# Kernel optimization log

Measured on AMD Instinct MI355X. Metric: run time of the kernel, lower is better.

Reference implementation:

```python
import jax, jax.numpy as jnp
import numpy as np

N, T, NC, D = 256, 20, 1, 32
NF, Q, VSTEPS, HDYN = 16, 32, 10, 256
HDIM = NF * 64           # n_filt * 4**3
DT = 0.1
BETA = 1.0
LOG2PI = float(np.log(2.0 * np.pi))


def conv2d(x, w, b):
    # k=4, s=2, p=1 : halves spatial dims. x: [B,Cin,H,W], w: [Cout,Cin,4,4]
    y = jax.lax.conv_general_dilated(x, w, (2, 2), [(1, 1), (1, 1)],
                                     dimension_numbers=('NCHW', 'OIHW', 'NCHW'))
    return y + b[None, :, None, None]


def deconv2d(x, w, b):
    # stride-2 transposed conv, doubles spatial dims. w: [Cout,Cin,4,4]
    y = jax.lax.conv_transpose(x, w, (2, 2), 'SAME',
                               dimension_numbers=('NCHW', 'OIHW', 'NCHW'))
    return y + b[None, :, None, None]


def encode(x, C1, c1, C2, c2, C3, c3, Wm, bm, Wl, bl):
    h = jax.nn.relu(conv2d(x, C1, c1))
    h = jax.nn.relu(conv2d(h, C2, c2))
    h = jax.nn.relu(conv2d(h, C3, c3))   # [B, 4*NF, 4, 4]
    h = h.reshape(h.shape[0], -1)        # [B, HDIM]
    return h @ Wm + bm, h @ Wl + bl


def setup_inputs() -> dict:
    key = jax.random.key(0)
    ks = jax.random.split(key, 40)
    r = lambda i, shape, s=0.05: s * jax.random.normal(ks[i], shape, jnp.float32)
    inp = {
        'X': jax.random.uniform(ks[0], (N, T, NC, D, D), jnp.float32),
        'eps_s0': jax.random.normal(ks[1], (N, Q), jnp.float32),
        'eps_v0': jax.random.normal(ks[2], (N, Q), jnp.float32),
        # enc_s (input = 1 frame)
        'Cs1': r(3, (NF, NC, 4, 4)), 'cs1': jnp.zeros((NF,)),
        'Cs2': r(4, (2 * NF, NF, 4, 4)), 'cs2': jnp.zeros((2 * NF,)),
        'Cs3': r(5, (4 * NF, 2 * NF, 4, 4)), 'cs3': jnp.zeros((4 * NF,)),
        'Wsm': r(6, (HDIM, Q)), 'bsm': jnp.zeros((Q,)),
        'Wsl': r(7, (HDIM, Q), 0.01), 'bsl': -1.0 * jnp.ones((Q,)),
        # enc_v (input = v_steps frames stacked as channels)
        'Cv1': r(8, (NF, VSTEPS * NC, 4, 4)), 'cv1': jnp.zeros((NF,)),
        'Cv2': r(9, (2 * NF, NF, 4, 4)), 'cv2': jnp.zeros((2 * NF,)),
        'Cv3': r(10, (4 * NF, 2 * NF, 4, 4)), 'cv3': jnp.zeros((4 * NF,)),
        'Wvm': r(11, (HDIM, Q)), 'bvm': jnp.zeros((Q,)),
        'Wvl': r(12, (HDIM, Q), 0.01), 'bvl': -1.0 * jnp.ones((Q,)),
        # dynamics f : R^{2q} -> R^q (tanh MLP)
        'W1': r(13, (2 * Q, HDYN), 0.1), 'b1': jnp.zeros((HDYN,)),
        'W2': r(14, (HDYN, Q), 0.1), 'b2': jnp.zeros((Q,)),
        # fc3 + decoder
        'Wf': r(15, (Q, HDIM)), 'bf': jnp.zeros((HDIM,)),
        'D1': r(16, (2 * NF, 4 * NF, 4, 4)), 'd1': jnp.zeros((2 * NF,)),
        'D2': r(17, (NF, 2 * NF, 4, 4)), 'd2': jnp.zeros((NF,)),
        'D3': r(18, (NC, NF, 4, 4)), 'd3': jnp.zeros((NC,)),
        'Ndata': 10000,
    }
    return inp


def reference(X, eps_s0, eps_v0,
              Cs1, cs1, Cs2, cs2, Cs3, cs3, Wsm, bsm, Wsl, bsl,
              Cv1, cv1, Cv2, cv2, Cv3, cv3, Wvm, bvm, Wvl, bvl,
              W1, b1, W2, b2, Wf, bf, D1, d1, D2, d2, D3, d3, Ndata):
    Nb, Tt = X.shape[0], X.shape[1]
    # ---- encode z0 = [v0, s0]
    s0_mu, s0_lv = encode(X[:, 0], Cs1, cs1, Cs2, cs2, Cs3, cs3, Wsm, bsm, Wsl, bsl)
    xv = X[:, :VSTEPS].reshape(Nb, VSTEPS * NC, D, D)
    v0_mu, v0_lv = encode(xv, Cv1, cv1, Cv2, cv2, Cv3, cv3, Wvm, bvm, Wvl, bvl)
    s0 = s0_mu + eps_s0 * jnp.exp(s0_lv)
    v0 = v0_mu + eps_v0 * jnp.exp(v0_lv)
    # standard-normal density of the base noise (q dims each)
    logp0 = (-0.5 * jnp.sum(eps_s0 ** 2, -1) - 0.5 * Q * LOG2PI) + \
            (-0.5 * jnp.sum(eps_v0 ** 2, -1) - 0.5 * Q * LOG2PI)
    z0 = jnp.concatenate([v0, s0], axis=1)               # [N,2q]
    qz0_m = jnp.concatenate([v0_mu, s0_mu], axis=1)
    qz0_logv = jnp.concatenate([v0_lv, s0_lv], axis=1)

    # ---- augmented ODE rhs: dz = [f(z), v], dlogp = -tr(df/dv)
    # exact trace for the tanh MLP: J = W2^T diag(1-h^2) W1^T, so
    # tr_{i<q} J = (1-h^2) @ c with c_k = sum_{i<q} W1[i,k] * W2[k,i]
    c = jnp.sum(W1[:Q] * W2.T, axis=0)                   # [HDYN]

    def rhs(vs):
        h = jnp.tanh(vs @ W1 + b1)                       # [N,HDYN]
        dv = h @ W2 + b2                                 # [N,q]
        dvs = jnp.concatenate([dv, vs[:, :Q]], axis=1)   # [N,2q]
        tr = (1.0 - h * h) @ c                           # [N]
        return dvs, -tr

    def rk4_step(carry, _):
        z, lp = carry
        k1z, k1l = rhs(z)
        k2z, k2l = rhs(z + 0.5 * DT * k1z)
        k3z, k3l = rhs(z + 0.5 * DT * k2z)
        k4z, k4l = rhs(z + DT * k3z)
        z2 = z + (DT / 6.0) * (k1z + 2 * k2z + 2 * k3z + k4z)
        lp2 = lp + (DT / 6.0) * (k1l + 2 * k2l + 2 * k3l + k4l)
        return (z2, lp2), (z2, lp2)

    (_, _), (zs, lps) = jax.lax.scan(rk4_step, (z0, logp0), None, length=Tt - 1)
    zt = jnp.concatenate([z0[None], zs], axis=0)         # [T,N,2q]
    logp = jnp.concatenate([logp0[None], lps], axis=0)   # [T,N]
    ztL = jnp.transpose(zt, (1, 0, 2))[None]             # [1,N,T,2q] (L=1)
    logpL = logp.T[None]                                 # [1,N,T]

    # ---- decode positions s_t
    s = ztL[..., Q:].reshape(-1, Q) @ Wf + bf            # [N*T, HDIM]
    h = s.reshape(-1, 4 * NF, 4, 4)
    h = jax.nn.relu(deconv2d(h, D1, d1))                 # [N*T,2NF,8,8]
    h = jax.nn.relu(deconv2d(h, D2, d2))                 # [N*T,NF,16,16]
    Xrec = jax.nn.sigmoid(deconv2d(h, D3, d3))           # [N*T,NC,32,32]
    Xrec = Xrec.reshape(1, Nb, Tt, NC, D, D)

    # ---- ELBO
    log_pzt = -0.5 * jnp.sum(ztL ** 2, -1) - Q * LOG2PI  # N(0,I) over 2q dims
    kl_z = (logpL - log_pzt).sum(2).mean(0)              # [N]
    lhood_L = jnp.log(0.001 + Xrec) * X[None] + jnp.log(1.001 - Xrec) * (1.0 - X[None])
    lhood = lhood_L.sum((2, 3, 4, 5)).mean(0)            # [N]
    kl_w = 0.5 * (jnp.sum(W1 ** 2) + jnp.sum(W2 ** 2))
    Nd = jnp.float32(Ndata)
    lh = Nd * lhood.mean()
    klz = Nd * kl_z.mean()
    elbo = lh - klz - BETA * kl_w
    return Xrec, qz0_m, qz0_logv, ztL, elbo, lh, klz, BETA * kl_w


if __name__ == '__main__':
    outs = reference(**setup_inputs())
    print(outs[0].shape, float(outs[4]))
```

## Files before the change

kernel.cpp:

```cpp
#include <hip/hip_runtime.h>
#include <math.h>

#define N_S 256
#define T_S 20
#define D_S 32
#define NF_S 16
#define Q_S 32
#define HDYN_S 256
#define HDIM_S 1024
#define VSTEPS_S 10
#define DT_S 0.1f
#define LOG2PI_F 1.8378770664093453f

#define OUT_XREC 0
#define OUT_QM   5242880
#define OUT_QLV  5259264
#define OUT_ZT   5275648
#define OUT_SCAL 5603328

#define WS_A1    0
#define WS_A3    0
#define WS_WT1   0
#define WS_WT2   32768
#define WS_WT3   40960
#define WS_A2    1048576
#define WS_S0MU  1572864
#define WS_S0LV  1581056
#define WS_V0MU  1589248
#define WS_V0LV  1597440
#define WS_LOGP  1605632
#define WS_LHOOD 1610752
#define WS_KLZ   1611008
#define WS_KLW   1611264
#define WS_TC    1611520
#define TC_S1 (WS_TC + 0)
#define TC_V1 (WS_TC + 256)
#define TC_S2 (WS_TC + 2816)
#define TC_V2 (WS_TC + 11008)
#define TC_S3 (WS_TC + 19200)
#define TC_V3 (WS_TC + 51968)

__device__ inline void enc_tr(const float* __restrict__ src, float* __restrict__ dst,
                              int e, int CI, int CO) {
    int co = e % CO; int r = e / CO; int tap = r & 15; int ci = r >> 4;
    dst[e] = src[(co * CI + ci) * 16 + tap];
}
__device__ inline void dec_tr(const float* __restrict__ src, float* __restrict__ dst,
                              int e, int CI, int CO) {
    int co = e % CO; int r = e / CO; int ci = r % CI; int tap = r / CI;
    dst[e] = src[(co * CI + ci) * 16 + tap];
}

__global__ __launch_bounds__(256) void prep_enc(
    const float* __restrict__ Cs1, const float* __restrict__ Cv1,
    const float* __restrict__ Cs2, const float* __restrict__ Cv2,
    const float* __restrict__ Cs3, const float* __restrict__ Cv3,
    float* __restrict__ ws)
{
    int idx = blockIdx.x * 256 + threadIdx.x;
    if (blockIdx.x == 0) ws[WS_LHOOD + threadIdx.x] = 0.f;
    if (idx < 256)        enc_tr(Cs1, ws + TC_S1, idx,          1, 16);
    else if (idx < 2816)  enc_tr(Cv1, ws + TC_V1, idx - 256,   10, 16);
    else if (idx < 11008) enc_tr(Cs2, ws + TC_S2, idx - 2816,  16, 32);
    else if (idx < 19200) enc_tr(Cv2, ws + TC_V2, idx - 11008, 16, 32);
    else if (idx < 51968) enc_tr(Cs3, ws + TC_S3, idx - 19200, 32, 64);
    else if (idx < 84736) enc_tr(Cv3, ws + TC_V3, idx - 51968, 32, 64);
}

template<int CIN>
__global__ __launch_bounds__(256) void conv1_lds(
    const float* __restrict__ x, const float* __restrict__ wt,
    const float* __restrict__ bias, float* __restrict__ out)
{
    __shared__ float xin[CIN * 630];
    __shared__ float wl[CIN * 256];
    __shared__ float bl[16];
    int b = blockIdx.x, yh = blockIdx.y, t = threadIdx.x;
    for (int e = t; e < CIN * 576; e += 256) {
        int ci = e / 576;
        int r = (e >> 5) - ci * 18;
        int cx = e & 31;
        int gy = yh * 16 - 1 + r;
        float v = (gy >= 0 && gy < 32) ? x[(size_t)b * 20480 + ci * 1024 + gy * 32 + cx] : 0.f;
        xin[ci * 630 + r * 35 + cx + 1] = v;
    }
    for (int e = t; e < CIN * 18; e += 256) {
        int ci = e / 18, r = e - ci * 18;
        xin[ci * 630 + r * 35 + 0] = 0.f;
        xin[ci * 630 + r * 35 + 33] = 0.f;
    }
    for (int e = t; e < CIN * 256; e += 256) wl[e] = wt[e];
    if (t < 16) bl[t] = bias[t];
    __syncthreads();

    int ocq = t >> 7, p = t & 127;
    int oyl = p >> 4, ox = p & 15;
    float acc[8];
    #pragma unroll
    for (int j = 0; j < 8; j++) acc[j] = bl[ocq * 8 + j];
    for (int ci = 0; ci < CIN; ci++) {
        const float* xc = xin + ci * 630;
        const float* wc = wl + ci * 256 + ocq * 8;
        #pragma unroll
        for (int ky = 0; ky < 4; ky++) {
            const float* xr = xc + (2 * oyl + ky) * 35;
            #pragma unroll
            for (int kx = 0; kx < 4; kx++) {
                float v = xr[2 * ox + kx];
                const float4* w4 = (const float4*)(wc + (ky * 4 + kx) * 16);
                float4 wa = w4[0], wb = w4[1];
                acc[0] = fmaf(v, wa.x, acc[0]);
                acc[1] = fmaf(v, wa.y, acc[1]);
                acc[2] = fmaf(v, wa.z, acc[2]);
                acc[3] = fmaf(v, wa.w, acc[3]);
                acc[4] = fmaf(v, wb.x, acc[4]);
                acc[5] = fmaf(v, wb.y, acc[5]);
                acc[6] = fmaf(v, wb.z, acc[6]);
                acc[7] = fmaf(v, wb.w, acc[7]);
            }
        }
    }
    int oy = yh * 8 + oyl;
    size_t ob = (size_t)b * 4096 + (size_t)(ocq * 8) * 256 + oy * 16 + ox;
    #pragma unroll
    for (int j = 0; j < 8; j++) out[ob + (size_t)j * 256] = fmaxf(acc[j], 0.f);
}

__global__ __launch_bounds__(256) void conv2_lds(
    const float* __restrict__ a1, const float* __restrict__ wt,
    const float* __restrict__ bias, float* __restrict__ out)
{
    __shared__ float xin[16 * 272];
    __shared__ float wl[4096];
    __shared__ float bl[16];
    int b = blockIdx.x, h = blockIdx.y, t = threadIdx.x;
    for (int e = t; e < 4096; e += 256) {
        int ci = e >> 8, r = e & 255, iy = r >> 4, ix = r & 15;
        xin[ci * 272 + iy * 17 + ix] = a1[(size_t)b * 4096 + e];
    }
    for (int e = t; e < 4096; e += 256) {
        int ci = e >> 8, r = e & 255, tap = r >> 4, oc = r & 15;
        wl[e] = wt[ci * 512 + tap * 32 + h * 16 + oc];
    }
    if (t < 16) bl[t] = bias[h * 16 + t];
    __syncthreads();

    int ocq = t >> 6, p = t & 63;
    int pa = p >> 3, pb = p & 7;
    float acc[4];
    #pragma unroll
    for (int j = 0; j < 4; j++) acc[j] = bl[ocq * 4 + j];
    for (int ci = 0; ci < 16; ci++) {
        const float* xc = xin + ci * 272;
        const float* wc = wl + ci * 256 + ocq * 4;
        #pragma unroll
        for (int ky = 0; ky < 4; ky++) {
            int iy = 2 * pa - 1 + ky;
            if ((unsigned)iy >= 16u) continue;
            const float* xr = xc + iy * 17;
            #pragma unroll
            for (int kx = 0; kx < 4; kx++) {
                int ix = 2 * pb - 1 + kx;
                if ((unsigned)ix >= 16u) continue;
                float v = xr[ix];
                float4 wv = *(const float4*)(wc + (ky * 4 + kx) * 16);
                acc[0] = fmaf(v, wv.x, acc[0]);
                acc[1] = fmaf(v, wv.y, acc[1]);
                acc[2] = fmaf(v, wv.z, acc[2]);
                acc[3] = fmaf(v, wv.w, acc[3]);
            }
        }
    }
    size_t ob = (size_t)b * 2048 + (size_t)(h * 16 + ocq * 4) * 64 + pa * 8 + pb;
    #pragma unroll
    for (int j = 0; j < 4; j++) out[ob + (size_t)j * 64] = fmaxf(acc[j], 0.f);
}

__global__ __launch_bounds__(256) void conv3_lds(
    const float* __restrict__ a2, const float* __restrict__ wt,
    const float* __restrict__ bias, float* __restrict__ out)
{
    __shared__ float xin[32 * 72];
    __shared__ float wl[16384];
    __shared__ float bl[32];
    int b = blockIdx.x, h = blockIdx.y, t = threadIdx.x;
    for (int e = t; e < 2048; e += 256) {
        int ci = e >> 6, r = e & 63, iy = r >> 3, ix = r & 7;
        xin[ci * 72 + iy * 9 + ix] = a2[(size_t)b * 2048 + e];
    }
    for (int e4 = t; e4 < 4096; e4 += 256) {
        int grp = e4 >> 3, c4 = e4 & 7;
        ((float4*)wl)[e4] = ((const float4*)(wt + grp * 64 + h * 32))[c4];
    }
    if (t < 32) bl[t] = bias[h * 32 + t];
    __syncthreads();

    int ocq = t >> 4, p = t & 15;
    int pa = p >> 2, pb = p & 3;
    float a0 = bl[ocq * 2], a1 = bl[ocq * 2 + 1];
    for (int ci = 0; ci < 32; ci++) {
        const float* xc = xin + ci * 72;
        const float* wc = wl + ci * 512 + ocq * 2;
        #pragma unroll
        for (int ky = 0; ky < 4; ky++) {
            int iy = 2 * pa - 1 + ky;
            if ((unsigned)iy >= 8u) continue;
            const float* xr = xc + iy * 9;
            #pragma unroll
            for (int kx = 0; kx < 4; kx++) {
                int ix = 2 * pb - 1 + kx;
                if ((unsigned)ix >= 8u) continue;
                float v = xr[ix];
                float2 wv = *(const float2*)(wc + (ky * 4 + kx) * 32);
                a0 = fmaf(v, wv.x, a0);
                a1 = fmaf(v, wv.y, a1);
            }
        }
    }
    size_t ob = (size_t)b * 1024 + (size_t)(h * 32 + ocq * 2) * 16 + pa * 4 + pb;
    out[ob] = fmaxf(a0, 0.f);
    out[ob + 16] = fmaxf(a1, 0.f);
}

__global__ __launch_bounds__(256) void fc_enc2(
    const float* __restrict__ h,
    const float* __restrict__ Wm, const float* __restrict__ bm,
    const float* __restrict__ Wl, const float* __restrict__ bl,
    float* __restrict__ mu, float* __restrict__ lv)
{
    __shared__ float pm[8][32], pl[8][32];
    int b = blockIdx.x, t = threadIdx.x;
    int q = t & 31, c = t >> 5;
    const float* hb = h + (size_t)b * HDIM_S + c * 128;
    const float* wmp = Wm + (c * 128) * Q_S + q;
    const float* wlp = Wl + (c * 128) * Q_S + q;
    float am = 0.f, al = 0.f;
    #pragma unroll 4
    for (int k = 0; k < 128; k++) {
        float hv = hb[k];
        am = fmaf(hv, wmp[k * Q_S], am);
        al = fmaf(hv, wlp[k * Q_S], al);
    }
    pm[c][q] = am; pl[c][q] = al;
    __syncthreads();
    if (t < 32) {
        float s = bm[t];
        #pragma unroll
        for (int c2 = 0; c2 < 8; c2++) s += pm[c2][t];
        mu[b * Q_S + t] = s;
    } else if (t < 64) {
        int qq = t - 32;
        float s = bl[qq];
        #pragma unroll
        for (int c2 = 0; c2 < 8; c2++) s += pl[c2][qq];
        lv[b * Q_S + qq] = s;
    }
}

__global__ __launch_bounds__(256) void reparam_prep(
    const float* __restrict__ s0mu, const float* __restrict__ s0lv,
    const float* __restrict__ v0mu, const float* __restrict__ v0lv,
    const float* __restrict__ eps_s, const float* __restrict__ eps_v,
    const float* __restrict__ D1, const float* __restrict__ D2,
    const float* __restrict__ D3,
    float* __restrict__ ws,
    float* __restrict__ qm, float* __restrict__ qlv,
    float* __restrict__ ztL, float* __restrict__ logp)
{
    int n = blockIdx.x, t = threadIdx.x;
    int idx = n * 256 + t;
    if (idx < 32768)      dec_tr(D1, ws + WS_WT1, idx,         64, 32);
    else if (idx < 40960) dec_tr(D2, ws + WS_WT2, idx - 32768, 32, 16);
    else if (idx < 41216) dec_tr(D3, ws + WS_WT3, idx - 40960, 16, 1);
    if (t < 64) {
        int q = t & 31;
        float mu, lvv, ep;
        if (t < 32) { mu = v0mu[n*32+q]; lvv = v0lv[n*32+q]; ep = eps_v[n*32+q]; }
        else        { mu = s0mu[n*32+q]; lvv = s0lv[n*32+q]; ep = eps_s[n*32+q]; }
        float zv = fmaf(ep, expf(lvv), mu);
        qm[n*64 + t]  = mu;
        qlv[n*64 + t] = lvv;
        ztL[(size_t)n * T_S * 64 + t] = zv;
        float e2 = ep * ep;
        #pragma unroll
        for (int off = 32; off; off >>= 1) e2 += __shfl_down(e2, off, 64);
        if (t == 0) logp[n * T_S] = -0.5f * e2 - Q_S * LOG2PI_F;
    }
}

__global__ __launch_bounds__(256) void ode_kernel(
    const float* __restrict__ W1, const float* __restrict__ b1,
    const float* __restrict__ W2, const float* __restrict__ b2,
    float* __restrict__ ztL, float* __restrict__ logp)
{
    __shared__ float W2s[HDYN_S * Q_S];
    __shared__ float zeval[64];
    __shared__ float hsh[HDYN_S];
    __shared__ float dvred[HDYN_S];
    __shared__ float red4[4];
    int n = blockIdx.x;
    int t = threadIdx.x;

    for (int i = t; i < HDYN_S * Q_S; i += 256) W2s[i] = W2[i];
    float w1r[64];
    #pragma unroll
    for (int j = 0; j < 64; j++) w1r[j] = W1[j * HDYN_S + t];
    float b1r = b1[t];
    __syncthreads();
    float ck = 0.f;
    #pragma unroll
    for (int i = 0; i < Q_S; i++) ck = fmaf(w1r[i], W2s[t * Q_S + i], ck);

    size_t zoff = (size_t)n * T_S * 64;
    float zj = 0.f, ksumj = 0.f, zevalj = 0.f, lp = 0.f, lsum = 0.f;
    if (t < 64) { zj = ztL[zoff + t]; zevalj = zj; zeval[t] = zj; }
    if (t == 0) lp = logp[n * T_S];

    const float wc[4] = {1.f, 2.f, 2.f, 1.f};
    const float ac[3] = {0.5f * DT_S, 0.5f * DT_S, DT_S};

    for (int step = 1; step < T_S; step++) {
        for (int e = 0; e < 4; e++) {
            __syncthreads();
            float p0 = 0.f, p1 = 0.f, p2 = 0.f, p3 = 0.f;
            #pragma unroll
            for (int j = 0; j < 16; j++) {
                p0 = fmaf(zeval[j],      w1r[j],      p0);
                p1 = fmaf(zeval[j + 16], w1r[j + 16], p1);
                p2 = fmaf(zeval[j + 32], w1r[j + 32], p2);
                p3 = fmaf(zeval[j + 48], w1r[j + 48], p3);
            }
            float pre = b1r + ((p0 + p1) + (p2 + p3));
            float hk = tanhf(pre);
            hsh[t] = hk;
            float gk = (1.f - hk * hk) * ck;
            #pragma unroll
            for (int off = 32; off; off >>= 1) gk += __shfl_down(gk, off, 64);
            if ((t & 63) == 0) red4[t >> 6] = gk;
            __syncthreads();
            {
                int i = t & 31, p = t >> 5;
                float a0 = 0.f, a1 = 0.f;
                #pragma unroll
                for (int kk = 0; kk < 16; kk++) {
                    a0 = fmaf(hsh[p * 32 + kk],      W2s[(p * 32 + kk) * Q_S + i],      a0);
                    a1 = fmaf(hsh[p * 32 + 16 + kk], W2s[(p * 32 + 16 + kk) * Q_S + i], a1);
                }
                dvred[t] = a0 + a1;
            }
            __syncthreads();
            if (t < 64) {
                float tr = red4[0] + red4[1] + red4[2] + red4[3];
                float zv_shfl = __shfl(zevalj, (t >= 32) ? (t - 32) : t, 64);
                float kzv;
                if (t < 32) {
                    float dvi = b2[t];
                    #pragma unroll
                    for (int p = 0; p < 8; p++) dvi += dvred[p * 32 + t];
                    kzv = dvi;
                } else kzv = zv_shfl;
                if (e == 0) ksumj = kzv; else ksumj = fmaf(wc[e], kzv, ksumj);
                if (t == 0) { float kl = -tr; lsum = (e == 0) ? kl : fmaf(wc[e], kl, lsum); }
                if (e < 3) {
                    zevalj = fmaf(ac[e], kzv, zj);
                    zeval[t] = zevalj;
                } else {
                    zj = fmaf(DT_S / 6.f, ksumj, zj);
                    zevalj = zj; zeval[t] = zj;
                    ztL[zoff + step * 64 + t] = zj;
                    if (t == 0) { lp = fmaf(DT_S / 6.f, lsum, lp); logp[n * T_S + step] = lp; }
                }
            }
        }
    }
}

__global__ __launch_bounds__(256) void decoder5(
    const float* __restrict__ ztL, const float* __restrict__ Wf, const float* __restrict__ bf,
    const float* __restrict__ wt1, const float* __restrict__ d1,
    const float* __restrict__ wt2, const float* __restrict__ d2,
    const float* __restrict__ wt3, const float* __restrict__ d3,
    const float* __restrict__ X, float* __restrict__ Xrec, float* __restrict__ lhood)
{
    __shared__ float zs[32];
    __shared__ float regA[3600];
    __shared__ float regB[4160];
    __shared__ float sh4[4];
    float* slp = regB;
    float* h2f = regB;
    float* h1f = regA;
    float* xst = regA;
    const int bidx = blockIdx.x;
    const int t = threadIdx.x;
    const int wu = __builtin_amdgcn_readfirstlane(t >> 6);
    const int l = t & 63;
    const int py = wu >> 1, px = wu & 1;

    if (t < 32) zs[t] = ztL[(size_t)bidx * 64 + 32 + t];
    {
        float4 z4 = make_float4(0.f, 0.f, 0.f, 0.f);
        for (int e = t; e < 678; e += 256) ((float4*)regB)[e] = z4;
        for (int e = t; e < 900; e += 256) ((float4*)regA)[e] = z4;
    }
    __syncthreads();

    {
        float4 acc = ((const float4*)bf)[t];
        const float4* Wf4 = (const float4*)Wf;
        #pragma unroll 4
        for (int q = 0; q < 32; q++) {
            float zq = zs[q];
            float4 wv = Wf4[q * 256 + t];
            acc.x = fmaf(zq, wv.x, acc.x);
            acc.y = fmaf(zq, wv.y, acc.y);
            acc.z = fmaf(zq, wv.z, acc.z);
            acc.w = fmaf(zq, wv.w, acc.w);
        }
        int k0 = t * 4;
        int ci = k0 >> 4;
        int iy = t & 3;
        float vv[4] = {acc.x, acc.y, acc.z, acc.w};
        #pragma unroll
        for (int j = 0; j < 4; j++)
            slp[(iy + 1) * 452 + (j + 1) * 72 + ci] = vv[j];
    }
    __syncthreads();

    {
        int ocq = l >> 3;
        int pp = l & 7;
        int a_ = pp >> 1, b2 = pp & 1;
        float acc0[4], acc1[4];
        #pragma unroll
        for (int j = 0; j < 4; j++) { acc0[j] = d1[ocq * 4 + j]; acc1[j] = acc0[j]; }
        #pragma unroll
        for (int sy = 0; sy < 2; sy++) {
            int ky = py + 2 * sy;
            int iy = a_ + py + sy - 1;
            #pragma unroll
            for (int sx = 0; sx < 2; sx++) {
                int kx = px + 2 * sx;
                int ix0 = 2 * b2 + px + sx - 1;
                const float4* ip0 = (const float4*)(slp + (iy + 1) * 452 + (ix0 + 1) * 72);
                const float4* ip1 = (const float4*)((const float*)ip0 + 72);
                const float* wb = wt1 + (ky * 4 + kx) * 2048 + ocq * 4;
                #pragma unroll 4
                for (int cc = 0; cc < 16; cc++) {
                    float4 va = ip0[cc];
                    float4 vb = ip1[cc];
                    float av[4] = {va.x, va.y, va.z, va.w};
                    float bv[4] = {vb.x, vb.y, vb.z, vb.w};
                    #pragma unroll
                    for (int r = 0; r < 4; r++) {
                        float4 wv = *(const float4*)(wb + (cc * 4 + r) * 32);
                        acc0[0] = fmaf(av[r], wv.x, acc0[0]); acc1[0] = fmaf(bv[r], wv.x, acc1[0]);
                        acc0[1] = fmaf(av[r], wv.y, acc0[1]); acc1[1] = fmaf(bv[r], wv.y, acc1[1]);
                        acc0[2] = fmaf(av[r], wv.z, acc0[2]); acc1[2] = fmaf(bv[r], wv.z, acc1[2]);
                        acc0[3] = fmaf(av[r], wv.w, acc0[3]); acc1[3] = fmaf(bv[r], wv.w, acc1[3]);
                    }
                }
            }
        }
        int y = 2 * a_ + py;
        int x0 = 4 * b2 + px;
        float4 r0, r1;
        r0.x = fmaxf(acc0[0],0.f); r0.y = fmaxf(acc0[1],0.f); r0.z = fmaxf(acc0[2],0.f); r0.w = fmaxf(acc0[3],0.f);
        r1.x = fmaxf(acc1[0],0.f); r1.y = fmaxf(acc1[1],0.f); r1.z = fmaxf(acc1[2],0.f); r1.w = fmaxf(acc1[3],0.f);
        *(float4*)(h1f + (y + 1) * 360 + (x0 + 1) * 36 + ocq * 4) = r0;
        *(float4*)(h1f + (y + 1) * 360 + (x0 + 3) * 36 + ocq * 4) = r1;
    }
    __syncthreads();

    {
        int a = l >> 3, b = l & 7;
        float acc[16];
        #pragma unroll
        for (int j = 0; j < 16; j++) acc[j] = d2[j];
        #pragma unroll
        for (int sy = 0; sy < 2; sy++) {
            int ky = py + 2 * sy;
            int iyf = a + py + sy - 1;
            #pragma unroll
            for (int sx = 0; sx < 2; sx++) {
                int kx = px + 2 * sx;
                int ixf = b + px + sx - 1;
                const float4* ip4 = (const float4*)(h1f + (iyf + 1) * 360 + (ixf + 1) * 36);
                const float* wb = wt2 + (ky * 4 + kx) * 512;
                #pragma unroll 2
                for (int cc = 0; cc < 8; cc++) {
                    float4 v = ip4[cc];
                    float vv[4] = {v.x, v.y, v.z, v.w};
                    #pragma unroll
                    for (int r = 0; r < 4; r++) {
                        const float4* wq = (const float4*)(wb + (cc * 4 + r) * 16);
                        float4 w0 = wq[0], w1 = wq[1], w2 = wq[2], w3 = wq[3];
                        float vr = vv[r];
                        acc[0]  = fmaf(vr, w0.x, acc[0]);
                        acc[1]  = fmaf(vr, w0.y, acc[1]);
                        acc[2]  = fmaf(vr, w0.z, acc[2]);
                        acc[3]  = fmaf(vr, w0.w, acc[3]);
                        acc[4]  = fmaf(vr, w1.x, acc[4]);
                        acc[5]  = fmaf(vr, w1.y, acc[5]);
                        acc[6]  = fmaf(vr, w1.z, acc[6]);
                        acc[7]  = fmaf(vr, w1.w, acc[7]);
                        acc[8]  = fmaf(vr, w2.x, acc[8]);
                        acc[9]  = fmaf(vr, w2.y, acc[9]);
                        acc[10] = fmaf(vr, w2.z, acc[10]);
                        acc[11] = fmaf(vr, w2.w, acc[11]);
                        acc[12] = fmaf(vr, w3.x, acc[12]);
                        acc[13] = fmaf(vr, w3.y, acc[13]);
                        acc[14] = fmaf(vr, w3.z, acc[14]);
                        acc[15] = fmaf(vr, w3.w, acc[15]);
                    }
                }
            }
        }
        __syncthreads();
        float* hq = h2f + (2 * a + py) * 260 + (2 * b + px) * 16;
        #pragma unroll
        for (int j = 0; j < 4; j++) {
            float4 r;
            r.x = fmaxf(acc[j*4+0], 0.f);
            r.y = fmaxf(acc[j*4+1], 0.f);
            r.z = fmaxf(acc[j*4+2], 0.f);
            r.w = fmaxf(acc[j*4+3], 0.f);
            *(float4*)(hq + j * 4) = r;
        }
    }
    __syncthreads();

    {
        int oy2 = l >> 2, b3 = l & 3;
        float acc[4];
        float d30 = d3[0];
        #pragma unroll
        for (int k = 0; k < 4; k++) acc[k] = d30;
        #pragma unroll
        for (int sy = 0; sy < 2; sy++) {
            int ky = py + 2 * sy;
            int iy = oy2 + py + sy - 1;
            if ((unsigned)iy >= 16u) continue;
            #pragma unroll
            for (int sx = 0; sx < 2; sx++) {
                int kx = px + 2 * sx;
                int cx = px + sx - 1;
                const float* wvp = wt3 + (ky * 4 + kx) * 16;
                #pragma unroll
                for (int k = 0; k < 4; k++) {
                    int ix = b3 + 4 * k + cx;
                    if ((unsigned)ix >= 16u) continue;
                    const float4* in4 = (const float4*)(h2f + iy * 260 + ix * 16);
                    #pragma unroll
                    for (int cc = 0; cc < 4; cc++) {
                        float4 v = in4[cc];
                        float4 wq = ((const float4*)wvp)[cc];
                        acc[k] = fmaf(v.x, wq.x, acc[k]);
                        acc[k] = fmaf(v.y, wq.y, acc[k]);
                        acc[k] = fmaf(v.z, wq.z, acc[k]);
                        acc[k] = fmaf(v.w, wq.w, acc[k]);
                    }
                }
            }
        }
        int oy = 2 * oy2 + py;
        #pragma unroll
        for (int k = 0; k < 4; k++) {
            int ox = 2 * (b3 + 4 * k) + px;
            xst[oy * 36 + ox] = 1.f / (1.f + expf(-acc[k]));
        }
    }
    __syncthreads();

    {
        int row = t >> 3, col = (t & 7) * 4;
        float4 xr4 = *(const float4*)(xst + row * 36 + col);
        *(float4*)(Xrec + (size_t)bidx * 1024 + t * 4) = xr4;
        float4 xi4 = *(const float4*)(X + (size_t)bidx * 1024 + t * 4);
        float ll = 0.f;
        ll += logf(0.001f + xr4.x) * xi4.x + logf(1.001f - xr4.x) * (1.f - xi4.x);
        ll += logf(0.001f + xr4.y) * xi4.y + logf(1.001f - xr4.y) * (1.f - xi4.y);
        ll += logf(0.001f + xr4.z) * xi4.z + logf(1.001f - xr4.z) * (1.f - xi4.z);
        ll += logf(0.001f + xr4.w) * xi4.w + logf(1.001f - xr4.w) * (1.f - xi4.w);
        #pragma unroll
        for (int off = 32; off; off >>= 1) ll += __shfl_down(ll, off, 64);
        if ((t & 63) == 0) sh4[t >> 6] = ll;
    }
    __syncthreads();
    if (t == 0) atomicAdd(&lhood[bidx / T_S], sh4[0] + sh4[1] + sh4[2] + sh4[3]);
}

__global__ __launch_bounds__(64) void klz_kernel(
    const float* __restrict__ ztL, const float* __restrict__ logp, float* __restrict__ klz)
{
    int n = blockIdx.x, t = threadIdx.x;
    float v = 0.f;
    if (t < T_S) {
        const float* z = ztL + ((size_t)n * T_S + t) * 64;
        float s2 = 0.f;
        #pragma unroll
        for (int j = 0; j < 64; j++) s2 = fmaf(z[j], z[j], s2);
        v = logp[n * T_S + t] - (-0.5f * s2 - Q_S * LOG2PI_F);
    }
    #pragma unroll
    for (int off = 32; off; off >>= 1) v += __shfl_down(v, off, 64);
    if (t == 0) klz[n] = v;
}

__global__ __launch_bounds__(256) void final2(
    const float* __restrict__ lhood, const float* __restrict__ klz,
    const float* __restrict__ W1, const float* __restrict__ W2,
    const int* __restrict__ Ndata, float* __restrict__ outs)
{
    __shared__ float shA[4], shB[4], shC[4];
    int t = threadIdx.x;
    float a = lhood[t];
    float b = klz[t];
    float c = 0.f;
    for (int i = t; i < 64 * HDYN_S; i += 256) c = fmaf(W1[i], W1[i], c);
    for (int i = t; i < HDYN_S * Q_S; i += 256) c = fmaf(W2[i], W2[i], c);
    #pragma unroll
    for (int off = 32; off; off >>= 1) {
        a += __shfl_down(a, off, 64);
        b += __shfl_down(b, off, 64);
        c += __shfl_down(c, off, 64);
    }
    if ((t & 63) == 0) { shA[t >> 6] = a; shB[t >> 6] = b; shC[t >> 6] = c; }
    __syncthreads();
    if (t == 0) {
        float Nd = (float)Ndata[0];
        float lh = Nd * ((shA[0] + shA[1] + shA[2] + shA[3]) / 256.f);
        float kz = Nd * ((shB[0] + shB[1] + shB[2] + shB[3]) / 256.f);
        float bkw = 0.5f * (shC[0] + shC[1] + shC[2] + shC[3]);
        outs[0] = lh - kz - bkw;
        outs[1] = lh;
        outs[2] = kz;
        outs[3] = bkw;
    }
}

extern "C" void kernel_launch(void* const* d_in, const int* in_sizes, int n_in,
                              void* d_out, int out_size, void* d_ws, size_t ws_size,
                              hipStream_t stream) {
    const float* X      = (const float*)d_in[0];
    const float* eps_s0 = (const float*)d_in[1];
    const float* eps_v0 = (const float*)d_in[2];
    const float* Cs1 = (const float*)d_in[3],  *cs1 = (const float*)d_in[4];
    const float* Cs2 = (const float*)d_in[5],  *cs2 = (const float*)d_in[6];
    const float* Cs3 = (const float*)d_in[7],  *cs3 = (const float*)d_in[8];
    const float* Wsm = (const float*)d_in[9],  *bsm = (const float*)d_in[10];
    const float* Wsl = (const float*)d_in[11], *bsl = (const float*)d_in[12];
    const float* Cv1 = (const float*)d_in[13], *cv1 = (const float*)d_in[14];
    const float* Cv2 = (const float*)d_in[15], *cv2 = (const float*)d_in[16];
    const float* Cv3 = (const float*)d_in[17], *cv3 = (const float*)d_in[18];
    const float* Wvm = (const float*)d_in[19], *bvm = (const float*)d_in[20];
    const float* Wvl = (const float*)d_in[21], *bvl = (const float*)d_in[22];
    const float* W1  = (const float*)d_in[23], *b1  = (const float*)d_in[24];
    const float* W2  = (const float*)d_in[25], *b2  = (const float*)d_in[26];
    const float* Wf  = (const float*)d_in[27], *bf  = (const float*)d_in[28];
    const float* D1  = (const float*)d_in[29], *d1  = (const float*)d_in[30];
    const float* D2  = (const float*)d_in[31], *d2  = (const float*)d_in[32];
    const float* D3  = (const float*)d_in[33], *d3  = (const float*)d_in[34];
    const int*   Ndata = (const int*)d_in[35];

    float* out = (float*)d_out;
    float* ws  = (float*)d_ws;

    prep_enc<<<331, 256, 0, stream>>>(Cs1, Cv1, Cs2, Cv2, Cs3, Cv3, ws);

    conv1_lds<1><<<dim3(256, 2), 256, 0, stream>>>(X, ws + TC_S1, cs1, ws + WS_A1);
    conv2_lds<<<dim3(256, 2), 256, 0, stream>>>(ws + WS_A1, ws + TC_S2, cs2, ws + WS_A2);
    conv3_lds<<<dim3(256, 2), 256, 0, stream>>>(ws + WS_A2, ws + TC_S3, cs3, ws + WS_A3);
    fc_enc2<<<256, 256, 0, stream>>>(ws + WS_A3, Wsm, bsm, Wsl, bsl, ws + WS_S0MU, ws + WS_S0LV);

    conv1_lds<10><<<dim3(256, 2), 256, 0, stream>>>(X, ws + TC_V1, cv1, ws + WS_A1);
    conv2_lds<<<dim3(256, 2), 256, 0, stream>>>(ws + WS_A1, ws + TC_V2, cv2, ws + WS_A2);
    conv3_lds<<<dim3(256, 2), 256, 0, stream>>>(ws + WS_A2, ws + TC_V3, cv3, ws + WS_A3);
    fc_enc2<<<256, 256, 0, stream>>>(ws + WS_A3, Wvm, bvm, Wvl, bvl, ws + WS_V0MU, ws + WS_V0LV);

    reparam_prep<<<256, 256, 0, stream>>>(ws + WS_S0MU, ws + WS_S0LV, ws + WS_V0MU, ws + WS_V0LV,
                                          eps_s0, eps_v0, D1, D2, D3, ws,
                                          out + OUT_QM, out + OUT_QLV,
                                          out + OUT_ZT, ws + WS_LOGP);

    ode_kernel<<<256, 256, 0, stream>>>(W1, b1, W2, b2, out + OUT_ZT, ws + WS_LOGP);

    decoder5<<<5120, 256, 0, stream>>>(out + OUT_ZT, Wf, bf,
                                       ws + WS_WT1, d1, ws + WS_WT2, d2, ws + WS_WT3, d3,
                                       X, out + OUT_XREC, ws + WS_LHOOD);

    klz_kernel<<<256, 64, 0, stream>>>(out + OUT_ZT, ws + WS_LOGP, ws + WS_KLZ);
    final2<<<1, 256, 0, stream>>>(ws + WS_LHOOD, ws + WS_KLZ, W1, W2, Ndata,
                                  out + OUT_SCAL);
}
```

Before: 609.5 us.

## Fold decoder linear layer into first deconvolution as precomputed affine map

Because the linear layer Wf and the first transposed conv D1 are both linear with no activation between them, a new prep kernel precomputes their composition as a 32-to-2048 matrix M1 plus a combined bias c1. Each decoder block then computes the first deconv output directly from the 32-dim latent with 8x32 FMAs per thread, instead of running the 32x1024 FC and then the 64-channel deconv. This also drops the slp staging buffer, its zero fill and one barrier. In exchange, the decoder reads a 256 KB M1 matrix per block from cache, and floating-point summation order changes.

```diff
diff --git a/kernel.cpp b/kernel.cpp
--- a/kernel.cpp
+++ b/kernel.cpp
@@ -20,10 +20,11 @@
 
 #define WS_A1    0
 #define WS_A3    0
-#define WS_WT1   0
 #define WS_WT2   32768
 #define WS_WT3   40960
 #define WS_A2    1048576
+#define WS_M1    1048576
+#define WS_C1    1114112
 #define WS_S0MU  1572864
 #define WS_S0LV  1581056
 #define WS_V0MU  1589248
@@ -257,21 +258,100 @@
     }
 }
 
+__global__ __launch_bounds__(256) void m1_prep(
+    const float* __restrict__ Wf, const float* __restrict__ bf,
+    const float* __restrict__ D1, const float* __restrict__ d1,
+    float* __restrict__ ws)
+{
+    int blk = blockIdx.x, t = threadIdx.x;
+    if (blk < 64) {
+        __shared__ float WfL[4096];
+        __shared__ float D1L[4096];
+        int j = blk >> 3, q4 = blk & 7;
+        for (int e = t; e < 4096; e += 256) {
+            int qq = e >> 10, k = e & 1023;
+            WfL[e] = Wf[(size_t)(q4 * 4 + qq) * 1024 + k];
+        }
+        for (int e = t; e < 4096; e += 256) {
+            int ocg = e >> 10, r = e & 1023;
+            D1L[e] = D1[(size_t)(ocg * 8 + j) * 1024 + r];
+        }
+        __syncthreads();
+        int p = t & 63, ocg = t >> 6;
+        int y = p >> 3, x = p & 7;
+        float acc[4] = {0.f, 0.f, 0.f, 0.f};
+        #pragma unroll
+        for (int sy = 0; sy < 2; sy++) {
+            int ky = (y & 1) + 2 * sy;
+            int iy = ((y + ky) >> 1) - 1;
+            if ((unsigned)iy >= 4u) continue;
+            #pragma unroll
+            for (int sx = 0; sx < 2; sx++) {
+                int kx = (x & 1) + 2 * sx;
+                int ix = ((x + kx) >> 1) - 1;
+                if ((unsigned)ix >= 4u) continue;
+                const float* dl = D1L + ocg * 1024 + ky * 4 + kx;
+                const float* wl = WfL + iy * 4 + ix;
+                for (int ci = 0; ci < 64; ci++) {
+                    float wv = dl[ci * 16];
+                    int kb = ci * 16;
+                    acc[0] = fmaf(wl[kb],        wv, acc[0]);
+                    acc[1] = fmaf(wl[1024 + kb], wv, acc[1]);
+                    acc[2] = fmaf(wl[2048 + kb], wv, acc[2]);
+                    acc[3] = fmaf(wl[3072 + kb], wv, acc[3]);
+                }
+            }
+        }
+        float4 o4 = make_float4(acc[0], acc[1], acc[2], acc[3]);
+        ((float4*)(ws + WS_M1))[blk * 256 + t] = o4;
+    } else {
+        __shared__ float bfL[1024];
+        __shared__ float D1c[2048];
+        int bb = blk - 64;
+        for (int e = t; e < 1024; e += 256) bfL[e] = bf[e];
+        for (int e = t; e < 2048; e += 256) D1c[e] = D1[(size_t)bb * 2048 + e];
+        __syncthreads();
+        int oidx = t >> 1, half = t & 1;
+        int ocr = oidx >> 6, p = oidx & 63;
+        int y = p >> 3, x = p & 7;
+        float acc = 0.f;
+        #pragma unroll
+        for (int sy = 0; sy < 2; sy++) {
+            int ky = (y & 1) + 2 * sy;
+            int iy = ((y + ky) >> 1) - 1;
+            if ((unsigned)iy >= 4u) continue;
+            #pragma unroll
+            for (int sx = 0; sx < 2; sx++) {
+                int kx = (x & 1) + 2 * sx;
+                int ix = ((x + kx) >> 1) - 1;
+                if ((unsigned)ix >= 4u) continue;
+                const float* dl = D1c + ocr * 1024 + half * 512 + ky * 4 + kx;
+                const float* wl = bfL + half * 512 + iy * 4 + ix;
+                for (int cc = 0; cc < 32; cc++)
+                    acc = fmaf(wl[cc * 16], dl[cc * 16], acc);
+            }
+        }
+        acc += __shfl_down(acc, 1, 64);
+        if (half == 0) {
+            int oc = bb * 2 + ocr;
+            ws[WS_C1 + (oc & 7) * 256 + (oc >> 3) * 64 + p] = acc + d1[oc];
+        }
+    }
+}
+
 __global__ __launch_bounds__(256) void reparam_prep(
     const float* __restrict__ s0mu, const float* __restrict__ s0lv,
     const float* __restrict__ v0mu, const float* __restrict__ v0lv,
     const float* __restrict__ eps_s, const float* __restrict__ eps_v,
-    const float* __restrict__ D1, const float* __restrict__ D2,
-    const float* __restrict__ D3,
+    const float* __restrict__ D2, const float* __restrict__ D3,
     float* __restrict__ ws,
     float* __restrict__ qm, float* __restrict__ qlv,
     float* __restrict__ ztL, float* __restrict__ logp)
 {
     int n = blockIdx.x, t = threadIdx.x;
     int idx = n * 256 + t;
-    if (idx < 32768)      dec_tr(D1, ws + WS_WT1, idx,         64, 32);
-    else if (idx < 40960) dec_tr(D2, ws + WS_WT2, idx - 32768, 32, 16);
-    else if (idx < 41216) dec_tr(D3, ws + WS_WT3, idx - 40960, 16, 1);
+    if (idx < 8192)      dec_tr(D2, ws + WS_WT2, idx,        32, 16);
+    else if (idx < 8448) dec_tr(D3, ws + WS_WT3, idx - 8192, 16, 1);
     if (t < 64) {
         int q = t & 31;
         float mu, lvv, ep;
@@ -376,8 +456,7 @@
 }
 
 __global__ __launch_bounds__(256) void decoder5(
-    const float* __restrict__ ztL, const float* __restrict__ Wf, const float* __restrict__ bf,
-    const float* __restrict__ wt1, const float* __restrict__ d1,
+    const float* __restrict__ ztL, const float* __restrict__ M1L, const float* __restrict__ c1L,
     const float* __restrict__ wt2, const float* __restrict__ d2,
     const float* __restrict__ wt3, const float* __restrict__ d3,
     const float* __restrict__ X, float* __restrict__ Xrec, float* __restrict__ lhood)
@@ -386,7 +465,6 @@
     __shared__ float regA[3600];
     __shared__ float regB[4160];
     __shared__ float sh4[4];
-    float* slp = regB;
     float* h2f = regB;
     float* h1f = regA;
     float* xst = regA;
@@ -399,75 +477,34 @@
     if (t < 32) zs[t] = ztL[(size_t)bidx * 64 + 32 + t];
     {
         float4 z4 = make_float4(0.f, 0.f, 0.f, 0.f);
-        for (int e = t; e < 678; e += 256) ((float4*)regB)[e] = z4;
         for (int e = t; e < 900; e += 256) ((float4*)regA)[e] = z4;
     }
     __syncthreads();
 
     {
-        float4 acc = ((const float4*)bf)[t];
-        const float4* Wf4 = (const float4*)Wf;
-        #pragma unroll 4
-        for (int q = 0; q < 32; q++) {
-            float zq = zs[q];
-            float4 wv = Wf4[q * 256 + t];
-            acc.x = fmaf(zq, wv.x, acc.x);
-            acc.y = fmaf(zq, wv.y, acc.y);
-            acc.z = fmaf(zq, wv.z, acc.z);
-            acc.w = fmaf(zq, wv.w, acc.w);
-        }
-        int k0 = t * 4;
-        int ci = k0 >> 4;
-        int iy = t & 3;
-        float vv[4] = {acc.x, acc.y, acc.z, acc.w};
-        #pragma unroll
-        for (int j = 0; j < 4; j++)
-            slp[(iy + 1) * 452 + (j + 1) * 72 + ci] = vv[j];
-    }
-    __syncthreads();
-
-    {
-        int ocq = l >> 3;
-        int pp = l & 7;
-        int a_ = pp >> 1, b2 = pp & 1;
-        float acc0[4], acc1[4];
-        #pragma unroll
-        for (int j = 0; j < 4; j++) { acc0[j] = d1[ocq * 4 + j]; acc1[j] = acc0[j]; }
-        #pragma unroll
-        for (int sy = 0; sy < 2; sy++) {
-            int ky = py + 2 * sy;
-            int iy = a_ + py + sy - 1;
-            #pragma unroll
-            for (int sx = 0; sx < 2; sx++) {
-                int kx = px + 2 * sx;
-                int ix0 = 2 * b2 + px + sx - 1;
-                const float4* ip0 = (const float4*)(slp + (iy + 1) * 452 + (ix0 + 1) * 72);
-                const float4* ip1 = (const float4*)((const float*)ip0 + 72);
-                const float* wb = wt1 + (ky * 4 + kx) * 2048 + ocq * 4;
-                #pragma unroll 4
-                for (int cc = 0; cc < 16; cc++) {
-                    float4 va = ip0[cc];
-                    float4 vb = ip1[cc];
-                    float av[4] = {va.x, va.y, va.z, va.w};
-                    float bv[4] = {vb.x, vb.y, vb.z, vb.w};
-                    #pragma unroll
-                    for (int r = 0; r < 4; r++) {
-                        float4 wv = *(const float4*)(wb + (cc * 4 + r) * 32);
-                        acc0[0] = fmaf(av[r], wv.x, acc0[0]); acc1[0] = fmaf(bv[r], wv.x, acc1[0]);
-                        acc0[1] = fmaf(av[r], wv.y, acc0[1]); acc1[1] = fmaf(bv[r], wv.y, acc1[1]);
-                        acc0[2] = fmaf(av[r], wv.z, acc0[2]); acc1[2] = fmaf(bv[r], wv.z, acc1[2]);
-                        acc0[3] = fmaf(av[r], wv.w, acc0[3]); acc1[3] = fmaf(bv[r], wv.w, acc1[3]);
-                    }
-                }
-            }
-        }
-        int y = 2 * a_ + py;
-        int x0 = 4 * b2 + px;
+        float acc[8];
+        #pragma unroll
+        for (int j = 0; j < 8; j++) acc[j] = c1L[j * 256 + t];
+        const float4* M14 = (const float4*)M1L;
+        #pragma unroll
+        for (int q4 = 0; q4 < 8; q4++) {
+            float4 z4 = *(const float4*)(zs + q4 * 4);
+            #pragma unroll
+            for (int j = 0; j < 8; j++) {
+                float4 m = M14[(j * 8 + q4) * 256 + t];
+                acc[j] = fmaf(z4.x, m.x, fmaf(z4.y, m.y, fmaf(z4.z, m.z, fmaf(z4.w, m.w, acc[j]))));
+            }
+        }
+        int p = t & 63, ocg = t >> 6;
+        int y = p >> 3, x = p & 7;
+        float* hp = h1f + (y + 1) * 360 + (x + 1) * 36 + ocg * 8;
         float4 r0, r1;
-        r0.x = fmaxf(acc0[0],0.f); r0.y = fmaxf(acc0[1],0.f); r0.z = fmaxf(acc0[2],0.f); r0.w = fmaxf(acc0[3],0.f);
-        r1.x = fmaxf(acc1[0],0.f); r1.y = fmaxf(acc1[1],0.f); r1.z = fmaxf(acc1[2],0.f); r1.w = fmaxf(acc1[3],0.f);
-        *(float4*)(h1f + (y + 1) * 360 + (x0 + 1) * 36 + ocq * 4) = r0;
-        *(float4*)(h1f + (y + 1) * 360 + (x0 + 3) * 36 + ocq * 4) = r1;
+        r0.x = fmaxf(acc[0], 0.f); r0.y = fmaxf(acc[1], 0.f);
+        r0.z = fmaxf(acc[2], 0.f); r0.w = fmaxf(acc[3], 0.f);
+        r1.x = fmaxf(acc[4], 0.f); r1.y = fmaxf(acc[5], 0.f);
+        r1.z = fmaxf(acc[6], 0.f); r1.w = fmaxf(acc[7], 0.f);
+        *(float4*)(hp)     = r0;
+        *(float4*)(hp + 4) = r1;
     }
     __syncthreads();
 
@@ -515,7 +552,6 @@
                 }
             }
         }
-        __syncthreads();
         float* hq = h2f + (2 * a + py) * 260 + (2 * b + px) * 16;
         #pragma unroll
         for (int j = 0; j < 4; j++) {
@@ -677,15 +713,17 @@
     conv3_lds<<<dim3(256, 2), 256, 0, stream>>>(ws + WS_A2, ws + TC_V3, cv3, ws + WS_A3);
     fc_enc2<<<256, 256, 0, stream>>>(ws + WS_A3, Wvm, bvm, Wvl, bvl, ws + WS_V0MU, ws + WS_V0LV);
 
+    m1_prep<<<80, 256, 0, stream>>>(Wf, bf, D1, d1, ws);
+
     reparam_prep<<<256, 256, 0, stream>>>(ws + WS_S0MU, ws + WS_S0LV, ws + WS_V0MU, ws + WS_V0LV,
-                                          eps_s0, eps_v0, D1, D2, D3, ws,
+                                          eps_s0, eps_v0, D2, D3, ws,
                                           out + OUT_QM, out + OUT_QLV,
                                           out + OUT_ZT, ws + WS_LOGP);
 
     ode_kernel<<<256, 256, 0, stream>>>(W1, b1, W2, b2, out + OUT_ZT, ws + WS_LOGP);
 
-    decoder5<<<5120, 256, 0, stream>>>(out + OUT_ZT, Wf, bf,
-                                       ws + WS_WT1, d1, ws + WS_WT2, d2, ws + WS_WT3, d3,
+    decoder5<<<5120, 256, 0, stream>>>(out + OUT_ZT, ws + WS_M1, ws + WS_C1,
+                                       ws + WS_WT2, d2, ws + WS_WT3, d3,
                                        X, out + OUT_XREC, ws + WS_LHOOD);
 
     klz_kernel<<<256, 64, 0, stream>>>(out + OUT_ZT, ws + WS_LOGP, ws + WS_KLZ);
```

New measurement: 502.4 us. 1.21x faster.
